# Performance work log

Measured on AMD Instinct MI355X. Metric: run time of the kernel, lower is better.

Reference implementation:

```python
import jax, jax.numpy as jnp
import numpy as np

EPS = 1e-12  # torch F.normalize eps

def _l2norm(x, axis):
    n = jnp.linalg.norm(x, axis=axis, keepdims=True)
    return x / jnp.maximum(n, EPS)

def setup_inputs() -> dict:
    key = jax.random.key(0)
    ks = jax.random.split(key, 4)
    B, T, C, E, I = 2, 2048, 1024, 8, 2048
    return {
        "hidden_states": jax.random.normal(ks[0], (B, T, C), dtype=jnp.float32),
        "sim_matrix": jax.random.normal(ks[1], (C, E), dtype=jnp.float32),
        "gates": jnp.zeros((E,), dtype=jnp.float32),
        "temperature": jnp.float32(1.0),
        "experts_mask": jnp.ones((E,), dtype=jnp.float32),
        "w1": jax.random.normal(ks[2], (E, C, I), dtype=jnp.float32) * (1.0 / np.sqrt(C)),
        "w2": jax.random.normal(ks[3], (E, I, C), dtype=jnp.float32) * (1.0 / np.sqrt(I)),
        "min_experts": 2,
    }

def _gating(flat_h, sim_matrix, gates, temperature, experts_mask, min_experts):
    # flat_h: [N, C]
    logit_scale = jax.nn.sigmoid(temperature)
    logits = _l2norm(flat_h, -1) @ _l2norm(sim_matrix, 0)  # [N, E]
    logits = logits * experts_mask
    gated = jax.nn.relu(logits - gates * logit_scale)
    # GateSTE: forward hard threshold, backward identity
    act = gated + jax.lax.stop_gradient((gated > 0).astype(gated.dtype) - gated)
    # fallback: tokens with no active expert get top-min_experts by logits
    inactive = jnp.sum(act, axis=1) == 0  # [N]
    _, idx = jax.lax.top_k(logits, min_experts)  # [N, k]
    fallback = jnp.sum(jax.nn.one_hot(idx, logits.shape[1], dtype=act.dtype), axis=1) > 0  # [N, E] bool
    act = jnp.where(inactive[:, None] & fallback, jnp.asarray(1.0, act.dtype), act)
    return act, logits

def reference(hidden_states, sim_matrix, gates, temperature, experts_mask, w1, w2, min_experts):
    b, t, c = hidden_states.shape
    e = w1.shape[0]
    act, router_logits = _gating(hidden_states.reshape(b * t, c), sim_matrix, gates,
                                 temperature, experts_mask, min_experts)
    inter = jnp.einsum('btc,eci->btei', hidden_states, w1)
    inter = jax.nn.gelu(inter, approximate=False)
    expert_out = jnp.einsum('btei,eic->btec', inter, w2)
    mask = act.reshape(b, t, e)
    summed = jnp.sum(expert_out * mask[..., None], axis=-2)  # [b,t,c]
    num_act = jnp.clip(jnp.sum(mask, axis=-1, keepdims=True), 1, None)
    final = summed / num_act
    return final, router_logits, act
```

## Files before the change

### kernel.cpp

```cpp
#include <hip/hip_runtime.h>
#include <math.h>

typedef __bf16 bf16x8 __attribute__((ext_vector_type(8)));
typedef __bf16 bf16x4 __attribute__((ext_vector_type(4)));
typedef float  f32x4  __attribute__((ext_vector_type(4)));

#define NTOK 4096
#define CDIM 1024
#define EEXP 8
#define IDIM 2048

__device__ __forceinline__ void async_copy16(const __bf16* g, __bf16* l) {
  __builtin_amdgcn_global_load_lds((const __attribute__((address_space(1))) void*)g,
                                   (__attribute__((address_space(3))) void*)l,
                                   16, 0, 0);
}

__device__ __forceinline__ float gelu_f(float x) {
  float u = 0.7978845608028654f * fmaf(0.044715f * x * x, x, x);
  float ex = __expf(-2.f * fabsf(u));
  float th = copysignf((1.f - ex) / (1.f + ex), u);
  return 0.5f * x * (1.f + th);
}

__global__ __launch_bounds__(256) void gating_kernel(
    const float* __restrict__ h, const float* __restrict__ sim,
    const float* __restrict__ gates, const float* __restrict__ temp,
    const float* __restrict__ emask, const int* __restrict__ minexp,
    float* __restrict__ out_logits, float* __restrict__ out_act,
    float* __restrict__ inv_num, __bf16* __restrict__ hb)
{
  const int t = blockIdx.x, tid = threadIdx.x;
  float4 hv4 = ((const float4*)(h + (size_t)t * CDIM))[tid];
  float hv[4] = {hv4.x, hv4.y, hv4.z, hv4.w};
  bf16x4 hb4 = {(__bf16)hv[0], (__bf16)hv[1], (__bf16)hv[2], (__bf16)hv[3]};
  ((bf16x4*)(hb + (size_t)t * CDIM))[tid] = hb4;

  float d[EEXP], nn[EEXP];
  #pragma unroll
  for (int e = 0; e < EEXP; ++e) { d[e] = 0.f; nn[e] = 0.f; }
  float ss = 0.f;
  #pragma unroll
  for (int j = 0; j < 4; ++j) {
    ss = fmaf(hv[j], hv[j], ss);
    const float* sr = sim + (size_t)(tid * 4 + j) * EEXP;
    float4 s0 = ((const float4*)sr)[0];
    float4 s1 = ((const float4*)sr)[1];
    float sv[8] = {s0.x, s0.y, s0.z, s0.w, s1.x, s1.y, s1.z, s1.w};
    #pragma unroll
    for (int e = 0; e < EEXP; ++e) {
      d[e]  = fmaf(hv[j], sv[e], d[e]);
      nn[e] = fmaf(sv[e], sv[e], nn[e]);
    }
  }
  #pragma unroll
  for (int off = 32; off > 0; off >>= 1) {
    ss += __shfl_down(ss, off);
    #pragma unroll
    for (int e = 0; e < EEXP; ++e) {
      d[e]  += __shfl_down(d[e], off);
      nn[e] += __shfl_down(nn[e], off);
    }
  }
  __shared__ float red[4][20];
  const int wv = tid >> 6;
  if ((tid & 63) == 0) {
    red[wv][0] = ss;
    #pragma unroll
    for (int e = 0; e < EEXP; ++e) { red[wv][1 + e] = d[e]; red[wv][9 + e] = nn[e]; }
  }
  __syncthreads();
  if (tid == 0) {
    float sst = red[0][0] + red[1][0] + red[2][0] + red[3][0];
    float inv_h = 1.f / fmaxf(sqrtf(sst), 1e-12f);
    float ls = 1.f / (1.f + expf(-temp[0]));
    float logit[EEXP], act[EEXP];
    float cnt = 0.f;
    #pragma unroll
    for (int e = 0; e < EEXP; ++e) {
      float dot = red[0][1 + e] + red[1][1 + e] + red[2][1 + e] + red[3][1 + e];
      float nne = red[0][9 + e] + red[1][9 + e] + red[2][9 + e] + red[3][9 + e];
      float inv_s = 1.f / fmaxf(sqrtf(nne), 1e-12f);
      logit[e] = dot * inv_h * inv_s * emask[e];
      float g = logit[e] - gates[e] * ls;
      act[e] = (g > 0.f) ? 1.f : 0.f;
      cnt += act[e];
    }
    if (cnt == 0.f) {
      int k = minexp[0];
      if (k > EEXP) k = EEXP;
      bool used[EEXP];
      #pragma unroll
      for (int e = 0; e < EEXP; ++e) used[e] = false;
      for (int j = 0; j < k; ++j) {
        int best = -1; float bv = 0.f;
        for (int e = 0; e < EEXP; ++e)
          if (!used[e] && (best < 0 || logit[e] > bv)) { best = e; bv = logit[e]; }
        if (best >= 0) { used[best] = true; act[best] = 1.f; cnt += 1.f; }
      }
    }
    float num = fmaxf(cnt, 1.f);
    inv_num[t] = 1.f / num;
    #pragma unroll
    for (int e = 0; e < EEXP; ++e) {
      out_logits[(size_t)t * EEXP + e] = logit[e];
      out_act[(size_t)t * EEXP + e]   = act[e];
    }
  }
}

__global__ __launch_bounds__(64) void pack_kernel(
    const float* __restrict__ out_act, int* __restrict__ counts,
    unsigned short* __restrict__ perm)
{
  const int e = blockIdx.x;
  const int lane = threadIdx.x;
  const unsigned long long ltmask = (lane == 63) ? ~0ULL >> 1 : (1ULL << lane) - 1ULL;
  int base = 0;
  for (int i = 0; i < NTOK / 64; ++i) {
    int tok = i * 64 + lane;
    bool f = out_act[(size_t)tok * EEXP + e] > 0.f;
    unsigned long long m = __ballot(f);
    if (f) perm[e * NTOK + base + __popcll(m & ltmask)] = (unsigned short)tok;
    base += __popcll(m);
  }
  if (lane == 0) counts[e] = base;
}

__global__ __launch_bounds__(256) void transpose_f32_bf16(
    const float* __restrict__ in0, __bf16* __restrict__ out0, int R, int Cc,
    long sIn, long sOut)
{
  const float* in = in0 + (size_t)blockIdx.z * sIn;
  __bf16* out = out0 + (size_t)blockIdx.z * sOut;
  __shared__ __align__(16) __bf16 tile[64][72];
  const int tid = threadIdx.x;
  const int c0 = blockIdx.x * 64, r0 = blockIdx.y * 64;
  #pragma unroll
  for (int p = 0; p < 2; ++p) {
    int lin = p * 256 + tid;
    int r = lin >> 3, c8 = (lin & 7) * 8;
    const float* src = in + (size_t)(r0 + r) * Cc + c0 + c8;
    float4 v0 = ((const float4*)src)[0];
    float4 v1 = ((const float4*)src)[1];
    bf16x8 v = {(__bf16)v0.x, (__bf16)v0.y, (__bf16)v0.z, (__bf16)v0.w,
                (__bf16)v1.x, (__bf16)v1.y, (__bf16)v1.z, (__bf16)v1.w};
    *(bf16x8*)&tile[r][c8] = v;
  }
  __syncthreads();
  #pragma unroll
  for (int p = 0; p < 2; ++p) {
    int lin = p * 256 + tid;
    int oc = lin >> 3, j8 = (lin & 7) * 8;
    bf16x8 o;
    #pragma unroll
    for (int jj = 0; jj < 8; ++jj) o[jj] = tile[j8 + jj][oc];
    *(bf16x8*)(out + (size_t)(c0 + oc) * R + r0 + j8) = o;
  }
}

template <int MODE, int NN, int KK, int NB>
__global__ __launch_bounds__(512, 2) void gemm_pk(
    const __bf16* __restrict__ A0, const __bf16* __restrict__ B0,
    const int* __restrict__ counts, const unsigned short* __restrict__ perm,
    const float* __restrict__ inv_num, void* __restrict__ Cout)
{
  const int hid = blockIdx.x;
  const int xr = hid & 7, q2 = hid >> 3;
  const int mb = q2 & 15;
  const int panel = ((q2 >> 4) << 3) + xr;
  const int e = panel / NB;
  const int nb = panel - e * NB;
  const int Me = counts[e];
  const int m0 = mb * 256;
  if (m0 >= Me) return;
  const int n0 = nb * 256;

  const int tid = threadIdx.x;
  const int wave = tid >> 6, lane = tid & 63;
  const int wr = wave >> 2, wc = wave & 3;
  const int quad = lane >> 4, lrow = lane & 15;
  const int sw0 = ((quad ^ (lrow & 7)) << 3);
  const int sw1 = (((4 + quad) ^ (lrow & 7)) << 3);

  __shared__ __align__(16) __bf16 lds[2 * 32768];

  const int lr2 = tid >> 3;
  const int ch  = (((tid & 7) ^ (lr2 & 7)) << 3);
  const unsigned short* pe = perm + e * NTOK;
  const __bf16* aP[4];
  const __bf16* bP[4];
  if (MODE == 0) {
    #pragma unroll
    for (int g = 0; g < 4; ++g)
      aP[g] = A0 + (size_t)pe[min(m0 + g * 64 + lr2, Me - 1)] * KK + ch;
  } else {
    const __bf16* Ab = A0 + (size_t)e * NTOK * KK;
    #pragma unroll
    for (int g = 0; g < 4; ++g)
      aP[g] = Ab + (size_t)(m0 + g * 64 + lr2) * KK + ch;
  }
  const __bf16* Bb = B0 + (size_t)e * ((size_t)CDIM * IDIM);
  #pragma unroll
  for (int g = 0; g < 4; ++g)
    bP[g] = Bb + (size_t)(n0 + g * 64 + lr2) * KK + ch;

  f32x4 acc[8][4] = {};
  constexpr int NS = KK / 64;

  {
    __bf16* slot = lds;
    #pragma unroll
    for (int g = 0; g < 4; ++g)
      async_copy16(aP[g], slot + g * 4096 + wave * 512);
    #pragma unroll
    for (int g = 0; g < 4; ++g)
      async_copy16(bP[g], slot + 16384 + g * 4096 + wave * 512);
  }
  asm volatile("s_waitcnt vmcnt(0)" ::: "memory");
  __builtin_amdgcn_s_barrier();

  const int arow0 = (wr << 7) + lrow;
  const int brow0 = (wc << 6) + lrow;

  for (int s = 0; s < NS; ++s) {
    if (s + 1 < NS) {
      __bf16* slot = lds + (((s + 1) & 1) << 15);
      const int ko = (s + 1) * 64;
      #pragma unroll
      for (int g = 0; g < 4; ++g)
        async_copy16(aP[g] + ko, slot + g * 4096 + wave * 512);
      #pragma unroll
      for (int g = 0; g < 4; ++g)
        async_copy16(bP[g] + ko, slot + 16384 + g * 4096 + wave * 512);
    }
    const __bf16* Asl = lds + ((s & 1) << 15);
    const __bf16* Bsl = Asl + 16384;
    #pragma unroll
    for (int kh = 0; kh < 2; ++kh) {
      const int sw = kh ? sw1 : sw0;
      bf16x8 bfr[4];
      #pragma unroll
      for (int ni = 0; ni < 4; ++ni)
        bfr[ni] = *(const bf16x8*)(Bsl + ((brow0 + ni * 16) << 6) + sw);
      #pragma unroll
      for (int mh = 0; mh < 2; ++mh) {
        bf16x8 af[4];
        #pragma unroll
        for (int mi = 0; mi < 4; ++mi)
          af[mi] = *(const bf16x8*)(Asl + ((arow0 + (mh * 4 + mi) * 16) << 6) + sw);
        __builtin_amdgcn_s_setprio(1);
        #pragma unroll
        for (int mi = 0; mi < 4; ++mi)
          #pragma unroll
          for (int ni = 0; ni < 4; ++ni)
            acc[mh * 4 + mi][ni] =
                __builtin_amdgcn_mfma_f32_16x16x32_bf16(af[mi], bfr[ni], acc[mh * 4 + mi][ni], 0, 0, 0);
        __builtin_amdgcn_s_setprio(0);
      }
    }
    if (s + 1 < NS) {
      asm volatile("s_waitcnt vmcnt(0)" ::: "memory");
      __builtin_amdgcn_s_barrier();
    }
  }

  if (MODE == 0) {
    __bf16* O = (__bf16*)Cout + (size_t)e * NTOK * NN;
    #pragma unroll
    for (int mi = 0; mi < 8; ++mi) {
      #pragma unroll
      for (int r = 0; r < 4; ++r) {
        const int row = m0 + (wr << 7) + mi * 16 + (quad << 2) + r;
        const float sv = inv_num[pe[min(row, Me - 1)]];
        #pragma unroll
        for (int ni = 0; ni < 4; ++ni) {
          const int col = n0 + (wc << 6) + ni * 16 + lrow;
          O[(size_t)row * NN + col] = (__bf16)(gelu_f(acc[mi][ni][r]) * sv);
        }
      }
    }
  } else {
    float* O = (float*)Cout;
    #pragma unroll
    for (int mi = 0; mi < 8; ++mi) {
      #pragma unroll
      for (int r = 0; r < 4; ++r) {
        const int row = m0 + (wr << 7) + mi * 16 + (quad << 2) + r;
        if (row < Me) {
          const int tok = pe[row];
          #pragma unroll
          for (int ni = 0; ni < 4; ++ni) {
            const int col = n0 + (wc << 6) + ni * 16 + lrow;
            atomicAdd(&O[(size_t)tok * NN + col], acc[mi][ni][r]);
          }
        }
      }
    }
  }
}

extern "C" void kernel_launch(void* const* d_in, const int* in_sizes, int n_in,
                              void* d_out, int out_size, void* d_ws, size_t ws_size,
                              hipStream_t stream) {
  (void)in_sizes; (void)n_in; (void)out_size; (void)ws_size;
  const float* h     = (const float*)d_in[0];
  const float* sim   = (const float*)d_in[1];
  const float* gates = (const float*)d_in[2];
  const float* temp  = (const float*)d_in[3];
  const float* emask = (const float*)d_in[4];
  const float* w1    = (const float*)d_in[5];
  const float* w2    = (const float*)d_in[6];
  const int*   minexp = (const int*)d_in[7];

  float* out_final  = (float*)d_out;
  float* out_logits = out_final + (size_t)NTOK * CDIM;
  float* out_act    = out_logits + (size_t)NTOK * EEXP;

  char* ws = (char*)d_ws;
  float*          inv_num  = (float*)(ws + 0);
  int*            counts   = (int*)(ws + 16384);
  unsigned short* perm     = (unsigned short*)(ws + 16448);
  __bf16*         hb       = (__bf16*)(ws + 81984);
  __bf16*         w1T_all  = (__bf16*)(ws + 8470592);
  __bf16*         w2T_all  = (__bf16*)(ws + 42025024);
  __bf16*         inter_pk = (__bf16*)(ws + 75579456);

  const long sW = (long)CDIM * IDIM;

  hipMemsetAsync(out_final, 0, (size_t)NTOK * CDIM * sizeof(float), stream);
  transpose_f32_bf16<<<dim3(IDIM / 64, CDIM / 64, EEXP), 256, 0, stream>>>(
      w1, w1T_all, CDIM, IDIM, sW, sW);
  transpose_f32_bf16<<<dim3(CDIM / 64, IDIM / 64, EEXP), 256, 0, stream>>>(
      w2, w2T_all, IDIM, CDIM, sW, sW);
  gating_kernel<<<NTOK, 256, 0, stream>>>(h, sim, gates, temp, emask, minexp,
                                          out_logits, out_act, inv_num, hb);
  pack_kernel<<<EEXP, 64, 0, stream>>>(out_act, counts, perm);
  gemm_pk<0, IDIM, CDIM, IDIM / 256><<<dim3((IDIM / 256) * (NTOK / 256) * EEXP), 512, 0, stream>>>(
      hb, w1T_all, counts, perm, inv_num, (void*)inter_pk);
  gemm_pk<1, CDIM, IDIM, CDIM / 256><<<dim3((CDIM / 256) * (NTOK / 256) * EEXP), 512, 0, stream>>>(
      inter_pk, w2T_all, counts, perm, inv_num, (void*)out_final);
}
```

Baseline: 500.4 us.

## Split K-stage loads into half-stages with finer-grained pipelined waits in grouped GEMM

Restructures the grouped expert GEMM main loop so each 64-wide K stage is split into two 32-wide halves, each with its own LDS region and swizzle layout. Global-to-LDS async copies for the next halves are issued between MFMA groups, with partial vmcnt waits and more frequent barriers in place of one full wait per stage. The aim is to overlap loads with MFMA work more finely and keep more copies in flight. In exchange it adds barriers, more complex wait-count bookkeeping, and new per-lane address math that must stay consistent with the new LDS layout.

After: 473.1 us. -5.5%, faster.

```diff
diff --git a/kernel.cpp b/kernel.cpp
--- a/kernel.cpp
+++ b/kernel.cpp
@@ -180,90 +180,99 @@
   const int wave = tid >> 6, lane = tid & 63;
   const int wr = wave >> 2, wc = wave & 3;
   const int quad = lane >> 4, lrow = lane & 15;
-  const int sw0 = ((quad ^ (lrow & 7)) << 3);
-  const int sw1 = (((4 + quad) ^ (lrow & 7)) << 3);
 
   __shared__ __align__(16) __bf16 lds[2 * 32768];
 
-  const int lr2 = tid >> 3;
-  const int ch  = (((tid & 7) ^ (lr2 & 7)) << 3);
+  const int sphys = (((lrow & 1) << 2) | quad) ^ ((lrow >> 1) & 7);
+  const int aro = ((((wr << 6) + (lrow >> 1)) << 6) + (sphys << 3));
+  const int bro = ((((wc << 5) + (lrow >> 1)) << 6) + (sphys << 3));
+
+  const int sst = (lane & 7) ^ (lane >> 3);
+  const int rb  = (wave << 4) + ((lane >> 3) << 1) + (sst >> 2);
+  const int cch = (sst & 3) << 3;
   const unsigned short* pe = perm + e * NTOK;
-  const __bf16* aP[4];
-  const __bf16* bP[4];
+  const __bf16 *aG0, *aG1;
   if (MODE == 0) {
-    #pragma unroll
-    for (int g = 0; g < 4; ++g)
-      aP[g] = A0 + (size_t)pe[min(m0 + g * 64 + lr2, Me - 1)] * KK + ch;
+    aG0 = A0 + (size_t)pe[min(m0 + rb, Me - 1)] * KK + cch;
+    aG1 = A0 + (size_t)pe[min(m0 + 128 + rb, Me - 1)] * KK + cch;
   } else {
     const __bf16* Ab = A0 + (size_t)e * NTOK * KK;
-    #pragma unroll
-    for (int g = 0; g < 4; ++g)
-      aP[g] = Ab + (size_t)(m0 + g * 64 + lr2) * KK + ch;
+    aG0 = Ab + (size_t)(m0 + rb) * KK + cch;
+    aG1 = Ab + (size_t)(m0 + 128 + rb) * KK + cch;
   }
   const __bf16* Bb = B0 + (size_t)e * ((size_t)CDIM * IDIM);
-  #pragma unroll
-  for (int g = 0; g < 4; ++g)
-    bP[g] = Bb + (size_t)(n0 + g * 64 + lr2) * KK + ch;
+  const __bf16* bG0 = Bb + (size_t)(n0 + rb) * KK + cch;
+  const __bf16* bG1 = Bb + (size_t)(n0 + 128 + rb) * KK + cch;
+
+#define STAGE_A(tt, khh) do { \
+    __bf16* _d = lds + (((tt) & 1) << 15) + ((khh) << 13) + (wave << 9); \
+    const size_t _co = (size_t)(tt) * 64 + (khh) * 32; \
+    async_copy16(aG0 + _co, _d); \
+    async_copy16(aG1 + _co, _d + 4096); \
+  } while (0)
+#define STAGE_B(tt, khh) do { \
+    __bf16* _d = lds + (((tt) & 1) << 15) + 16384 + ((khh) << 13) + (wave << 9); \
+    const size_t _co = (size_t)(tt) * 64 + (khh) * 32; \
+    async_copy16(bG0 + _co, _d); \
+    async_copy16(bG1 + _co, _d + 4096); \
+  } while (0)
+#define MFMA16(base) do { \
+    __builtin_amdgcn_s_setprio(1); \
+    _Pragma("unroll") \
+    for (int mi = 0; mi < 4; ++mi) \
+      _Pragma("unroll") \
+      for (int ni = 0; ni < 4; ++ni) \
+        acc[(base) + mi][ni] = __builtin_amdgcn_mfma_f32_16x16x32_bf16(af[mi], bfr[ni], acc[(base) + mi][ni], 0, 0, 0); \
+    __builtin_amdgcn_s_setprio(0); \
+  } while (0)
 
   f32x4 acc[8][4] = {};
   constexpr int NS = KK / 64;
 
-  {
-    __bf16* slot = lds;
-    #pragma unroll
-    for (int g = 0; g < 4; ++g)
-      async_copy16(aP[g], slot + g * 4096 + wave * 512);
-    #pragma unroll
-    for (int g = 0; g < 4; ++g)
-      async_copy16(bP[g], slot + 16384 + g * 4096 + wave * 512);
-  }
-  asm volatile("s_waitcnt vmcnt(0)" ::: "memory");
+  STAGE_A(0, 0); STAGE_B(0, 0);
+  STAGE_A(0, 1); STAGE_B(0, 1);
+  STAGE_A(1, 0); STAGE_B(1, 0);
+  asm volatile("s_waitcnt vmcnt(8)" ::: "memory");
   __builtin_amdgcn_s_barrier();
 
-  const int arow0 = (wr << 7) + lrow;
-  const int brow0 = (wc << 6) + lrow;
-
-  for (int s = 0; s < NS; ++s) {
-    if (s + 1 < NS) {
-      __bf16* slot = lds + (((s + 1) & 1) << 15);
-      const int ko = (s + 1) * 64;
-      #pragma unroll
-      for (int g = 0; g < 4; ++g)
-        async_copy16(aP[g] + ko, slot + g * 4096 + wave * 512);
-      #pragma unroll
-      for (int g = 0; g < 4; ++g)
-        async_copy16(bP[g] + ko, slot + 16384 + g * 4096 + wave * 512);
-    }
-    const __bf16* Asl = lds + ((s & 1) << 15);
-    const __bf16* Bsl = Asl + 16384;
-    #pragma unroll
-    for (int kh = 0; kh < 2; ++kh) {
-      const int sw = kh ? sw1 : sw0;
-      bf16x8 bfr[4];
-      #pragma unroll
-      for (int ni = 0; ni < 4; ++ni)
-        bfr[ni] = *(const bf16x8*)(Bsl + ((brow0 + ni * 16) << 6) + sw);
-      #pragma unroll
-      for (int mh = 0; mh < 2; ++mh) {
-        bf16x8 af[4];
-        #pragma unroll
-        for (int mi = 0; mi < 4; ++mi)
-          af[mi] = *(const bf16x8*)(Asl + ((arow0 + (mh * 4 + mi) * 16) << 6) + sw);
-        __builtin_amdgcn_s_setprio(1);
-        #pragma unroll
-        for (int mi = 0; mi < 4; ++mi)
-          #pragma unroll
-          for (int ni = 0; ni < 4; ++ni)
-            acc[mh * 4 + mi][ni] =
-                __builtin_amdgcn_mfma_f32_16x16x32_bf16(af[mi], bfr[ni], acc[mh * 4 + mi][ni], 0, 0, 0);
-        __builtin_amdgcn_s_setprio(0);
-      }
-    }
-    if (s + 1 < NS) {
-      asm volatile("s_waitcnt vmcnt(0)" ::: "memory");
-      __builtin_amdgcn_s_barrier();
-    }
-  }
+  for (int t = 0; t < NS; ++t) {
+    const __bf16* SA0 = lds + ((t & 1) << 15);
+    const __bf16* SA1 = SA0 + 8192;
+    const __bf16* SBk0 = SA0 + 16384;
+    const __bf16* SBk1 = SA0 + 24576;
+    bf16x8 af[4], bfr[4];
+    #pragma unroll
+    for (int ni = 0; ni < 4; ++ni) bfr[ni] = *(const bf16x8*)(SBk0 + bro + ni * 512);
+    #pragma unroll
+    for (int mi = 0; mi < 4; ++mi) af[mi] = *(const bf16x8*)(SA0 + aro + mi * 512);
+    if (t + 1 < NS) STAGE_A(t + 1, 1);
+    MFMA16(0);
+    __builtin_amdgcn_s_barrier();
+    #pragma unroll
+    for (int mi = 0; mi < 4; ++mi) af[mi] = *(const bf16x8*)(SA0 + aro + 2048 + mi * 512);
+    if (t + 1 < NS) STAGE_B(t + 1, 1);
+    MFMA16(4);
+    if (t + 1 < NS) { asm volatile("s_waitcnt vmcnt(8)" ::: "memory"); }
+    else            { asm volatile("s_waitcnt vmcnt(0)" ::: "memory"); }
+    __builtin_amdgcn_s_barrier();
+    #pragma unroll
+    for (int ni = 0; ni < 4; ++ni) bfr[ni] = *(const bf16x8*)(SBk1 + bro + ni * 512);
+    #pragma unroll
+    for (int mi = 0; mi < 4; ++mi) af[mi] = *(const bf16x8*)(SA1 + aro + mi * 512);
+    if (t + 2 < NS) STAGE_A(t + 2, 0);
+    MFMA16(0);
+    __builtin_amdgcn_s_barrier();
+    #pragma unroll
+    for (int mi = 0; mi < 4; ++mi) af[mi] = *(const bf16x8*)(SA1 + aro + 2048 + mi * 512);
+    if (t + 2 < NS) STAGE_B(t + 2, 0);
+    MFMA16(4);
+    if (t + 2 < NS)      { asm volatile("s_waitcnt vmcnt(8)" ::: "memory"); }
+    else if (t + 1 < NS) { asm volatile("s_waitcnt vmcnt(4)" ::: "memory"); }
+    __builtin_amdgcn_s_barrier();
+  }
+#undef STAGE_A
+#undef STAGE_B
+#undef MFMA16
 
   if (MODE == 0) {
     __bf16* O = (__bf16*)Cout + (size_t)e * NTOK * NN;
```

## Shrink grouped GEMM tiles to 128x128 with single-buffered LDS and 4 waves

Applied to the files above, without the earlier changes.

Changes the per-expert GEMM from 256x256 tiles with 8 waves and double-buffered LDS prefetch to 128x128 tiles with 4 waves and a single LDS buffer synchronized each k-step. Smaller tiles reduce padding waste for experts with few tokens and raise the block count and occupancy. In exchange, the overlap between global loads and MFMA is lost, operand reuse per tile drops, and the priority hints are removed.

Measured after the change: 501.9 us. No clear change (+0.3%).

```diff
diff --git a/kernel.cpp b/kernel.cpp
--- a/kernel.cpp
+++ b/kernel.cpp
@@ -160,118 +160,96 @@
 }
 
 template <int MODE, int NN, int KK, int NB>
-__global__ __launch_bounds__(512, 2) void gemm_pk(
+__global__ __launch_bounds__(256) void gemm_pk(
     const __bf16* __restrict__ A0, const __bf16* __restrict__ B0,
     const int* __restrict__ counts, const unsigned short* __restrict__ perm,
     const float* __restrict__ inv_num, void* __restrict__ Cout)
 {
   const int hid = blockIdx.x;
-  const int xr = hid & 7, q2 = hid >> 3;
-  const int mb = q2 & 15;
-  const int panel = ((q2 >> 4) << 3) + xr;
+  const int xr = hid & 7;
+  const int mb = (hid >> 3) & 31;
+  const int panel = ((hid >> 8) << 3) + xr;
   const int e = panel / NB;
   const int nb = panel - e * NB;
   const int Me = counts[e];
-  const int m0 = mb * 256;
+  const int m0 = mb * 128;
   if (m0 >= Me) return;
-  const int n0 = nb * 256;
+  const int n0 = nb * 128;
 
   const int tid = threadIdx.x;
   const int wave = tid >> 6, lane = tid & 63;
-  const int wr = wave >> 2, wc = wave & 3;
+  const int wr = wave >> 1, wc = wave & 1;
   const int quad = lane >> 4, lrow = lane & 15;
   const int sw0 = ((quad ^ (lrow & 7)) << 3);
-  const int sw1 = (((4 + quad) ^ (lrow & 7)) << 3);
-
-  __shared__ __align__(16) __bf16 lds[2 * 32768];
-
-  const int lr2 = tid >> 3;
-  const int ch  = (((tid & 7) ^ (lr2 & 7)) << 3);
+  const int sw1 = (((4 | quad) ^ (lrow & 7)) << 3);
+
+  __shared__ __align__(16) __bf16 As[8192];
+  __shared__ __align__(16) __bf16 Bs[8192];
+
+  const int rb = tid >> 3;
+  const int ch = (((tid & 7) ^ (rb & 7)) << 3);
   const unsigned short* pe = perm + e * NTOK;
   const __bf16* aP[4];
   const __bf16* bP[4];
   if (MODE == 0) {
     #pragma unroll
     for (int g = 0; g < 4; ++g)
-      aP[g] = A0 + (size_t)pe[min(m0 + g * 64 + lr2, Me - 1)] * KK + ch;
+      aP[g] = A0 + (size_t)pe[min(m0 + g * 32 + rb, Me - 1)] * KK + ch;
   } else {
     const __bf16* Ab = A0 + (size_t)e * NTOK * KK;
     #pragma unroll
     for (int g = 0; g < 4; ++g)
-      aP[g] = Ab + (size_t)(m0 + g * 64 + lr2) * KK + ch;
+      aP[g] = Ab + (size_t)(m0 + g * 32 + rb) * KK + ch;
   }
   const __bf16* Bb = B0 + (size_t)e * ((size_t)CDIM * IDIM);
   #pragma unroll
   for (int g = 0; g < 4; ++g)
-    bP[g] = Bb + (size_t)(n0 + g * 64 + lr2) * KK + ch;
-
-  f32x4 acc[8][4] = {};
+    bP[g] = Bb + (size_t)(n0 + g * 32 + rb) * KK + ch;
+
+  f32x4 acc[4][4] = {};
   constexpr int NS = KK / 64;
 
-  {
-    __bf16* slot = lds;
+  const int abase = ((wr << 6) + lrow) << 6;
+  const int bbase = ((wc << 6) + lrow) << 6;
+
+  for (int s = 0; s < NS; ++s) {
+    if (s) __syncthreads();
+    const int ko = s * 64;
     #pragma unroll
     for (int g = 0; g < 4; ++g)
-      async_copy16(aP[g], slot + g * 4096 + wave * 512);
+      async_copy16(aP[g] + ko, As + g * 2048 + wave * 512);
     #pragma unroll
     for (int g = 0; g < 4; ++g)
-      async_copy16(bP[g], slot + 16384 + g * 4096 + wave * 512);
-  }
-  asm volatile("s_waitcnt vmcnt(0)" ::: "memory");
-  __builtin_amdgcn_s_barrier();
-
-  const int arow0 = (wr << 7) + lrow;
-  const int brow0 = (wc << 6) + lrow;
-
-  for (int s = 0; s < NS; ++s) {
-    if (s + 1 < NS) {
-      __bf16* slot = lds + (((s + 1) & 1) << 15);
-      const int ko = (s + 1) * 64;
-      #pragma unroll
-      for (int g = 0; g < 4; ++g)
-        async_copy16(aP[g] + ko, slot + g * 4096 + wave * 512);
-      #pragma unroll
-      for (int g = 0; g < 4; ++g)
-        async_copy16(bP[g] + ko, slot + 16384 + g * 4096 + wave * 512);
-    }
-    const __bf16* Asl = lds + ((s & 1) << 15);
-    const __bf16* Bsl = Asl + 16384;
-    #pragma unroll
-    for (int kh = 0; kh < 2; ++kh) {
-      const int sw = kh ? sw1 : sw0;
-      bf16x8 bfr[4];
+      async_copy16(bP[g] + ko, Bs + g * 2048 + wave * 512);
+    __syncthreads();
+    bf16x8 a0[4], b0[4];
+    #pragma unroll
+    for (int mi = 0; mi < 4; ++mi) a0[mi] = *(const bf16x8*)(As + abase + mi * 1024 + sw0);
+    #pragma unroll
+    for (int ni = 0; ni < 4; ++ni) b0[ni] = *(const bf16x8*)(Bs + bbase + ni * 1024 + sw0);
+    #pragma unroll
+    for (int mi = 0; mi < 4; ++mi)
       #pragma unroll
       for (int ni = 0; ni < 4; ++ni)
-        bfr[ni] = *(const bf16x8*)(Bsl + ((brow0 + ni * 16) << 6) + sw);
-      #pragma unroll
-      for (int mh = 0; mh < 2; ++mh) {
-        bf16x8 af[4];
-        #pragma unroll
-        for (int mi = 0; mi < 4; ++mi)
-          af[mi] = *(const bf16x8*)(Asl + ((arow0 + (mh * 4 + mi) * 16) << 6) + sw);
-        __builtin_amdgcn_s_setprio(1);
-        #pragma unroll
-        for (int mi = 0; mi < 4; ++mi)
-          #pragma unroll
-          for (int ni = 0; ni < 4; ++ni)
-            acc[mh * 4 + mi][ni] =
-                __builtin_amdgcn_mfma_f32_16x16x32_bf16(af[mi], bfr[ni], acc[mh * 4 + mi][ni], 0, 0, 0);
-        __builtin_amdgcn_s_setprio(0);
-      }
-    }
-    if (s + 1 < NS) {
-      asm volatile("s_waitcnt vmcnt(0)" ::: "memory");
-      __builtin_amdgcn_s_barrier();
-    }
+        acc[mi][ni] = __builtin_amdgcn_mfma_f32_16x16x32_bf16(a0[mi], b0[ni], acc[mi][ni], 0, 0, 0);
+    #pragma unroll
+    for (int mi = 0; mi < 4; ++mi) a0[mi] = *(const bf16x8*)(As + abase + mi * 1024 + sw1);
+    #pragma unroll
+    for (int ni = 0; ni < 4; ++ni) b0[ni] = *(const bf16x8*)(Bs + bbase + ni * 1024 + sw1);
+    #pragma unroll
+    for (int mi = 0; mi < 4; ++mi)
+      #pragma unroll
+      for (int ni = 0; ni < 4; ++ni)
+        acc[mi][ni] = __builtin_amdgcn_mfma_f32_16x16x32_bf16(a0[mi], b0[ni], acc[mi][ni], 0, 0, 0);
   }
 
   if (MODE == 0) {
     __bf16* O = (__bf16*)Cout + (size_t)e * NTOK * NN;
     #pragma unroll
-    for (int mi = 0; mi < 8; ++mi) {
+    for (int mi = 0; mi < 4; ++mi) {
       #pragma unroll
       for (int r = 0; r < 4; ++r) {
-        const int row = m0 + (wr << 7) + mi * 16 + (quad << 2) + r;
+        const int row = m0 + (wr << 6) + mi * 16 + (quad << 2) + r;
         const float sv = inv_num[pe[min(row, Me - 1)]];
         #pragma unroll
         for (int ni = 0; ni < 4; ++ni) {
@@ -283,10 +261,10 @@
   } else {
     float* O = (float*)Cout;
     #pragma unroll
-    for (int mi = 0; mi < 8; ++mi) {
+    for (int mi = 0; mi < 4; ++mi) {
       #pragma unroll
       for (int r = 0; r < 4; ++r) {
-        const int row = m0 + (wr << 7) + mi * 16 + (quad << 2) + r;
+        const int row = m0 + (wr << 6) + mi * 16 + (quad << 2) + r;
         if (row < Me) {
           const int tok = pe[row];
           #pragma unroll
@@ -336,8 +314,8 @@
   gating_kernel<<<NTOK, 256, 0, stream>>>(h, sim, gates, temp, emask, minexp,
                                           out_logits, out_act, inv_num, hb);
   pack_kernel<<<EEXP, 64, 0, stream>>>(out_act, counts, perm);
-  gemm_pk<0, IDIM, CDIM, IDIM / 256><<<dim3((IDIM / 256) * (NTOK / 256) * EEXP), 512, 0, stream>>>(
+  gemm_pk<0, IDIM, CDIM, IDIM / 128><<<dim3((IDIM / 128) * (NTOK / 128) * EEXP), 256, 0, stream>>>(
       hb, w1T_all, counts, perm, inv_num, (void*)inter_pk);
-  gemm_pk<1, CDIM, IDIM, CDIM / 256><<<dim3((CDIM / 256) * (NTOK / 256) * EEXP), 512, 0, stream>>>(
+  gemm_pk<1, CDIM, IDIM, CDIM / 128><<<dim3((CDIM / 128) * (NTOK / 128) * EEXP), 256, 0, stream>>>(
       inter_pk, w2T_all, counts, perm, inv_num, (void*)out_final);
 }
```
